# Performance work log

Hardware: AMD Instinct MI355X
Metric: run time of the kernel (lower is better)

The kernel has to match this reference:

```python
import jax, jax.numpy as jnp
import numpy as np

TOPK = 20
BN_EPS = 1e-5
NEG_SLOPE = 0.2  # DGL GAT default leaky_relu slope


def setup_inputs() -> dict:
    B, N, Ft, D = 128, 512, 64, 64
    key = jax.random.key(0)
    ks = jax.random.split(key, 6)
    return {
        "data": jax.random.normal(ks[0], (B, N, Ft), jnp.float32),
        "emb": jax.random.normal(ks[1], (N, D), jnp.float32) * 0.5,
        "fc_w": jax.random.normal(ks[2], (D, Ft), jnp.float32) * (1.0 / np.sqrt(Ft)),
        "fc_b": jnp.zeros((D,), jnp.float32),
        "attn_w": jax.random.normal(ks[3], (4 * D,), jnp.float32) * (1.0 / np.sqrt(4 * D)),
        "attn_b": jnp.zeros((), jnp.float32),
        "bn_gamma": jnp.ones((D,), jnp.float32),
        "bn_beta": jnp.zeros((D,), jnp.float32),
        "out_w": jax.random.normal(ks[4], (D,), jnp.float32) * (1.0 / np.sqrt(D)),
        "out_b": jnp.zeros((), jnp.float32),
    }


def reference(data, emb, fc_w, fc_b, attn_w, attn_b, bn_gamma, bn_beta, out_w, out_b):
    B, N, Ft = data.shape
    D = emb.shape[-1]

    # --- dynamic graph build from detached embeddings (cosine-sim topk) ---
    w = jax.lax.stop_gradient(emb)
    nrm = jnp.linalg.norm(w, axis=-1)
    cos = (w @ w.T) / (nrm[:, None] * nrm[None, :])      # [N, N]
    _, topk_idx = jax.lax.top_k(cos, TOPK)               # [N, TOPK]
    src = topk_idx.reshape(-1)                           # gated_j (message sources)
    dst = jnp.tile(jnp.arange(N), TOPK)                  # gated_i = arange(N).repeat(1,topk).flatten()

    # --- GAT layer: z = W x + b ; edge score from concat([z, emb]) at both ends ---
    z = jnp.einsum("bnf,df->bnd", data, fc_w) + fc_b     # [B, N, D]
    key_feat = jnp.concatenate([z, jnp.broadcast_to(emb, (B, N, D))], axis=-1)  # [B, N, 2D]
    a_src, a_dst = attn_w[: 2 * D], attn_w[2 * D :]
    s_src = jnp.einsum("bnd,d->bn", key_feat, a_src)
    s_dst = jnp.einsum("bnd,d->bn", key_feat, a_dst)
    e = jax.nn.leaky_relu(s_src[:, src] + s_dst[:, dst] + attn_b, NEG_SLOPE)    # [B, E]

    # segment softmax over incoming edges of each dst node (same edges every batch)
    m = jnp.full((B, N), -jnp.inf, e.dtype).at[:, dst].max(e)
    p = jnp.exp(e - m[:, dst])
    denom = jnp.zeros((B, N), e.dtype).at[:, dst].add(p)
    alpha = p / denom[:, dst]                            # [B, E]

    # scatter-aggregate messages
    h = jnp.zeros_like(z).at[:, dst].add(alpha[..., None] * z[:, src])          # [B, N, D]

    # --- trailing dense: mul by embedding, BatchNorm1d over channel D, relu, linear ---
    rst = h * emb[None]                                  # [B, N, D]
    mu = rst.mean(axis=(0, 1))
    var = rst.var(axis=(0, 1))
    rst = jax.nn.relu((rst - mu) / jnp.sqrt(var + BN_EPS) * bn_gamma + bn_beta)
    out = jnp.einsum("bnd,d->bn", rst, out_w) + out_b    # [B, N]
    return out
```

## Files before the change

### kernel.cpp

```cpp
#include <hip/hip_runtime.h>
#include <hip/hip_bf16.h>

#define NN 512
#define DD 64
#define TOPK 20
#define BB 128

__global__ __launch_bounds__(256) void k1_topk(const float* __restrict__ emb,
                                               const float* __restrict__ attn_w,
                                               int* __restrict__ topk,
                                               float* __restrict__ es_src,
                                               float* __restrict__ es_dst,
                                               double* __restrict__ gstats) {
    __shared__ float4 lds4[2048];
    const int bid = blockIdx.x, t = threadIdx.x;
    const int wid = t >> 6, lane = t & 63;
    const int i = bid * 4 + wid;
    const float4* e4 = (const float4*)emb;

    if (bid == 0 && t < 128) gstats[t] = 0.0;

    float4 wif[16];
    #pragma unroll
    for (int c = 0; c < 16; ++c) wif[c] = e4[i * 16 + c];

    double di = 0.0;
    #pragma unroll
    for (int c = 0; c < 16; ++c) {
        double wx = wif[c].x, wy = wif[c].y, wz = wif[c].z, ww = wif[c].w;
        di += wx * wx; di += wy * wy; di += wz * wz; di += ww * ww;
    }

    double dot[8] = {0,0,0,0,0,0,0,0};
    double dj [8] = {0,0,0,0,0,0,0,0};

    for (int tile = 0; tile < 4; ++tile) {
        __syncthreads();
        for (int m = t; m < 2048; m += 256) {
            const int row = m >> 4, c = m & 15;
            lds4[row * 16 + (c ^ (row & 15))] = e4[tile * 2048 + m];
        }
        __syncthreads();
        #pragma unroll
        for (int rb = 0; rb < 2; ++rb) {
            const int slot = tile * 2 + rb;
            const int rl = rb * 64 + lane;
            const int rx = rl & 15;
            #pragma unroll
            for (int c = 0; c < 16; ++c) {
                float4 v = lds4[rl * 16 + (c ^ rx)];
                float4 w = wif[c];
                double vx = v.x, vy = v.y, vz = v.z, vw = v.w;
                dot[slot] += (double)w.x * vx; dot[slot] += (double)w.y * vy;
                dot[slot] += (double)w.z * vz; dot[slot] += (double)w.w * vw;
                dj [slot] += vx * vx; dj[slot] += vy * vy; dj[slot] += vz * vz; dj[slot] += vw * vw;
            }
        }
    }

    const double nrm_i = sqrt(di);
    double v[8];
    #pragma unroll
    for (int s = 0; s < 8; ++s) v[s] = dot[s] / (nrm_i * sqrt(dj[s]));

    for (int k = 0; k < TOPK; ++k) {
        double bv = v[0]; int bs = 0;
        #pragma unroll
        for (int s = 1; s < 8; ++s) if (v[s] > bv) { bv = v[s]; bs = s; }
        int bi = bs * 64 + lane;
        #pragma unroll
        for (int off = 32; off > 0; off >>= 1) {
            double ov = __shfl_xor(bv, off);
            int    oi = __shfl_xor(bi, off);
            if (ov > bv || (ov == bv && oi < bi)) { bv = ov; bi = oi; }
        }
        if (lane == 0) topk[i * TOPK + k] = bi;
        if ((bi & 63) == lane) v[bi >> 6] = -1e300;
    }

    float wf = emb[i * 64 + lane];
    float v1 = wf * attn_w[64 + lane];
    float v2 = wf * attn_w[192 + lane];
    #pragma unroll
    for (int off = 32; off > 0; off >>= 1) {
        v1 += __shfl_xor(v1, off);
        v2 += __shfl_xor(v2, off);
    }
    if (lane == 0) { es_src[i] = v1; es_dst[i] = v2; }
}

__global__ __launch_bounds__(256) void k2_gemm(const float* __restrict__ data,
                                               const float* __restrict__ fc_w,
                                               const float* __restrict__ fc_b,
                                               const float* __restrict__ attn_w,
                                               float* __restrict__ z,
                                               float* __restrict__ zsrc,
                                               float* __restrict__ zdst) {
    __shared__ float As [64][68];
    __shared__ float WsT[64][68];
    __shared__ float redA[64][17];
    __shared__ float redB[64][17];
    const int t = threadIdx.x;
    const long r0 = (long)blockIdx.x * 64;
    const float4* data4 = (const float4*)data;
    const float4* fcw4  = (const float4*)fc_w;

    for (int m = t; m < 1024; m += 256) {
        const int r = m >> 4, c4 = m & 15;
        *(float4*)&As[r][c4 * 4] = data4[(r0 + r) * 16 + c4];
    }
    for (int m = t; m < 1024; m += 256) {
        const int d = m >> 4, f4 = m & 15;
        float4 v = fcw4[d * 16 + f4];
        WsT[f4 * 4 + 0][d] = v.x;
        WsT[f4 * 4 + 1][d] = v.y;
        WsT[f4 * 4 + 2][d] = v.z;
        WsT[f4 * 4 + 3][d] = v.w;
    }
    __syncthreads();

    const int tr = t >> 4, tc = t & 15;
    float acc[4][4] = {};
    for (int k0 = 0; k0 < 64; k0 += 4) {
        float4 a4[4], b4[4];
        #pragma unroll
        for (int i = 0; i < 4; ++i) a4[i] = *(float4*)&As[tr * 4 + i][k0];
        #pragma unroll
        for (int kk = 0; kk < 4; ++kk) b4[kk] = *(float4*)&WsT[k0 + kk][tc * 4];
        #pragma unroll
        for (int i = 0; i < 4; ++i) {
            acc[i][0] += a4[i].x * b4[0].x + a4[i].y * b4[1].x + a4[i].z * b4[2].x + a4[i].w * b4[3].x;
            acc[i][1] += a4[i].x * b4[0].y + a4[i].y * b4[1].y + a4[i].z * b4[2].y + a4[i].w * b4[3].y;
            acc[i][2] += a4[i].x * b4[0].z + a4[i].y * b4[1].z + a4[i].z * b4[2].z + a4[i].w * b4[3].z;
            acc[i][3] += a4[i].x * b4[0].w + a4[i].y * b4[1].w + a4[i].z * b4[2].w + a4[i].w * b4[3].w;
        }
    }
    float bias[4], aw0[4], aw2[4];
    #pragma unroll
    for (int j = 0; j < 4; ++j) {
        bias[j] = fc_b[tc * 4 + j];
        aw0[j]  = attn_w[tc * 4 + j];
        aw2[j]  = attn_w[128 + tc * 4 + j];
    }
    #pragma unroll
    for (int i = 0; i < 4; ++i) {
        float zb[4];
        #pragma unroll
        for (int j = 0; j < 4; ++j) zb[j] = acc[i][j] + bias[j];
        float4 vv; vv.x = zb[0]; vv.y = zb[1]; vv.z = zb[2]; vv.w = zb[3];
        *(float4*)&z[(r0 + tr * 4 + i) * 64 + tc * 4] = vv;
        redA[tr * 4 + i][tc] = zb[0] * aw0[0] + zb[1] * aw0[1] + zb[2] * aw0[2] + zb[3] * aw0[3];
        redB[tr * 4 + i][tc] = zb[0] * aw2[0] + zb[1] * aw2[1] + zb[2] * aw2[2] + zb[3] * aw2[3];
    }
    __syncthreads();
    if (t < 64) {
        float sA = 0.f, sB = 0.f;
        #pragma unroll
        for (int k = 0; k < 16; ++k) { sA += redA[t][k]; sB += redB[t][k]; }
        zsrc[r0 + t] = sA;
        zdst[r0 + t] = sB;
    }
}

__global__ __launch_bounds__(256) void k3_attn(const float* __restrict__ z,
                                               const float* __restrict__ zsrc,
                                               const float* __restrict__ zdst,
                                               const float* __restrict__ es_src,
                                               const float* __restrict__ es_dst,
                                               const int* __restrict__ topk,
                                               const float* __restrict__ emb,
                                               const float* __restrict__ attn_b_p,
                                               float* __restrict__ rst,
                                               double* __restrict__ gstats) {
    __shared__ float  zs[512 * 16];
    __shared__ double alf_pool[2560];
    __shared__ unsigned short sIdx[256 * 20];
    float* alf = (float*)alf_pool;

    const int b    = blockIdx.x >> 2;
    const int dq   = blockIdx.x & 3;
    const int doff = dq * 16;
    const int t    = threadIdx.x;
    const float attn_b = *attn_b_p;
    const long b512 = (long)b * NN;

    float4* zs4 = (float4*)zs;
    for (int m = t; m < 2048; m += 256) {
        const int n = m >> 2, c4i = m & 3;
        zs4[m] = *(const float4*)(z + (b512 + n) * 64 + doff + c4i * 4);
    }
    __syncthreads();

    const int c4 = t & 3;
    const int rq = t >> 2;
    double s1[4] = {0,0,0,0}, s2[4] = {0,0,0,0};

    for (int chunk = 0; chunk < 2; ++chunk) {
        {
            const int n = chunk * 256 + t;
            const float sd = zdst[b512 + n] + es_dst[n] + attn_b;
            float ev[TOPK];
            float m0 = -1e30f;
            #pragma unroll
            for (int tt = 0; tt < TOPK; ++tt) {
                const int s = topk[n + tt * NN];
                sIdx[t * TOPK + tt] = (unsigned short)s;
                float e = zsrc[b512 + s] + es_src[s] + sd;
                e = (e >= 0.f) ? e : 0.2f * e;
                ev[tt] = e;
                m0 = fmaxf(m0, e);
            }
            float dsum = 0.f;
            #pragma unroll
            for (int tt = 0; tt < TOPK; ++tt) { ev[tt] = __expf(ev[tt] - m0); dsum += ev[tt]; }
            const float inv = 1.0f / dsum;
            #pragma unroll
            for (int tt = 0; tt < TOPK; ++tt) alf[t * TOPK + tt] = ev[tt] * inv;
        }
        __syncthreads();

        #pragma unroll
        for (int it = 0; it < 4; ++it) {
            const int nl = it * 64 + rq;
            const int n  = chunk * 256 + nl;
            float4 acc = {0.f, 0.f, 0.f, 0.f};
            #pragma unroll
            for (int tt = 0; tt < TOPK; ++tt) {
                const float a = alf[nl * TOPK + tt];
                const float4 zv = zs4[(int)sIdx[nl * TOPK + tt] * 4 + c4];
                acc.x += a * zv.x; acc.y += a * zv.y; acc.z += a * zv.z; acc.w += a * zv.w;
            }
            const float4 ev = *(const float4*)&emb[n * 64 + doff + c4 * 4];
            float4 r;
            r.x = acc.x * ev.x; r.y = acc.y * ev.y; r.z = acc.z * ev.z; r.w = acc.w * ev.w;
            *(float4*)&rst[(b512 + n) * 64 + doff + c4 * 4] = r;
            s1[0] += (double)r.x; s2[0] += (double)r.x * (double)r.x;
            s1[1] += (double)r.y; s2[1] += (double)r.y * (double)r.y;
            s1[2] += (double)r.z; s2[2] += (double)r.z * (double)r.z;
            s1[3] += (double)r.w; s2[3] += (double)r.w * (double)r.w;
        }
        __syncthreads();
    }

    double* r1 = alf_pool;
    double* r2 = alf_pool + 1024;
    #pragma unroll
    for (int j = 0; j < 4; ++j) {
        r1[(c4 * 4 + j) * 64 + rq] = s1[j];
        r2[(c4 * 4 + j) * 64 + rq] = s2[j];
    }
    __syncthreads();
    if (t < 16) {
        double a = 0.0, bb = 0.0;
        for (int q = 0; q < 64; ++q) { a += r1[t * 64 + q]; bb += r2[t * 64 + q]; }
        atomicAdd(&gstats[doff + t], a);
        atomicAdd(&gstats[64 + doff + t], bb);
    }
}

__global__ __launch_bounds__(256) void k5_out(const float* __restrict__ rst,
                                              const double* __restrict__ gstats,
                                              const float* __restrict__ gamma,
                                              const float* __restrict__ beta,
                                              const float* __restrict__ out_w,
                                              const float* __restrict__ out_b_p,
                                              float* __restrict__ out) {
    __shared__ float scv[64], biv[64];
    const int t = threadIdx.x;
    if (t < 64) {
        const double M = (double)BB * (double)NN;
        const double s  = gstats[t];
        const double s2 = gstats[64 + t];
        const double mu  = s / M;
        const double var = s2 / M - mu * mu;
        const float scale = (float)((double)gamma[t] / sqrt(var + 1e-5));
        scv[t] = scale;
        biv[t] = beta[t] - (float)mu * scale;
    }
    __syncthreads();

    const int wid = t >> 6, lane = t & 63;
    const float sc = scv[lane], bi = biv[lane], ow = out_w[lane];
    const float ob = *out_b_p;
    const long rowbase = (long)blockIdx.x * 16 + wid * 4;
    float v[4];
    #pragma unroll
    for (int rr = 0; rr < 4; ++rr)
        v[rr] = fmaxf(rst[(rowbase + rr) * 64 + lane] * sc + bi, 0.f) * ow;
    #pragma unroll
    for (int off = 32; off > 0; off >>= 1)
        #pragma unroll
        for (int rr = 0; rr < 4; ++rr) v[rr] += __shfl_down(v[rr], off);
    if (lane == 0)
        #pragma unroll
        for (int rr = 0; rr < 4; ++rr) out[rowbase + rr] = v[rr] + ob;
}

extern "C" void kernel_launch(void* const* d_in, const int* in_sizes, int n_in,
                              void* d_out, int out_size, void* d_ws, size_t ws_size,
                              hipStream_t stream) {
    const float* data   = (const float*)d_in[0];
    const float* emb    = (const float*)d_in[1];
    const float* fc_w   = (const float*)d_in[2];
    const float* fc_b   = (const float*)d_in[3];
    const float* attn_w = (const float*)d_in[4];
    const float* attn_b = (const float*)d_in[5];
    const float* gamma  = (const float*)d_in[6];
    const float* beta   = (const float*)d_in[7];
    const float* out_w  = (const float*)d_in[8];
    const float* out_b  = (const float*)d_in[9];
    float* out = (float*)d_out;

    char* ws = (char*)d_ws;
    float*  z      = (float*) (ws + 0);
    float*  rst    = (float*) (ws + 16777216);
    float*  zsrc   = (float*) (ws + 33554432);
    float*  zdst   = (float*) (ws + 33816576);
    int*    topk   = (int*)   (ws + 34078720);
    float*  es_src = (float*) (ws + 34119680);
    float*  es_dst = (float*) (ws + 34121728);
    double* gstats = (double*)(ws + 34123776);

    k1_topk<<<128, 256, 0, stream>>>(emb, attn_w, topk, es_src, es_dst, gstats);
    k2_gemm<<<1024, 256, 0, stream>>>(data, fc_w, fc_b, attn_w, z, zsrc, zdst);
    k3_attn<<<BB * 4, 256, 0, stream>>>(z, zsrc, zdst, es_src, es_dst, topk, emb,
                                        attn_b, rst, gstats);
    k5_out<<<4096, 256, 0, stream>>>(rst, gstats, gamma, beta, out_w, out_b, out);
}
```

Measured before the change: 162.6 us.

## Fuse top-k graph build and input GEMM into one heterogeneous launch

Merges the cosine-similarity top-k kernel and the fc GEMM kernel into one launch. The first 128 blocks build the graph and the remaining 512 blocks compute z. The GEMM is rewritten as one wave per 32 rows, with fc_w columns held in registers and data broadcast through readlane, and the z·attn reductions done by wave shuffles. The top-k LDS tile switches from an XOR swizzle to padded rows. This removes one launch and overlaps the two independent stages, at the cost of a long serial FMA chain per row and heavy register use (64-float Breg).

```diff
diff --git a/kernel.cpp b/kernel.cpp
--- a/kernel.cpp
+++ b/kernel.cpp
@@ -6,159 +6,145 @@
 #define TOPK 20
 #define BB 128
 
-__global__ __launch_bounds__(256) void k1_topk(const float* __restrict__ emb,
-                                               const float* __restrict__ attn_w,
-                                               int* __restrict__ topk,
-                                               float* __restrict__ es_src,
-                                               float* __restrict__ es_dst,
-                                               double* __restrict__ gstats) {
-    __shared__ float4 lds4[2048];
+__global__ __launch_bounds__(256) void L1_fused(const float* __restrict__ data,
+                                                const float* __restrict__ emb,
+                                                const float* __restrict__ fc_w,
+                                                const float* __restrict__ fc_b,
+                                                const float* __restrict__ attn_w,
+                                                float* __restrict__ z,
+                                                float* __restrict__ zsrc,
+                                                float* __restrict__ zdst,
+                                                int* __restrict__ topk,
+                                                float* __restrict__ es_src,
+                                                float* __restrict__ es_dst,
+                                                double* __restrict__ gstats) {
+    __shared__ __align__(16) char smem[34816];
     const int bid = blockIdx.x, t = threadIdx.x;
     const int wid = t >> 6, lane = t & 63;
-    const int i = bid * 4 + wid;
-    const float4* e4 = (const float4*)emb;
-
-    if (bid == 0 && t < 128) gstats[t] = 0.0;
-
-    float4 wif[16];
-    #pragma unroll
-    for (int c = 0; c < 16; ++c) wif[c] = e4[i * 16 + c];
-
-    double di = 0.0;
-    #pragma unroll
-    for (int c = 0; c < 16; ++c) {
-        double wx = wif[c].x, wy = wif[c].y, wz = wif[c].z, ww = wif[c].w;
-        di += wx * wx; di += wy * wy; di += wz * wz; di += ww * ww;
-    }
-
-    double dot[8] = {0,0,0,0,0,0,0,0};
-    double dj [8] = {0,0,0,0,0,0,0,0};
-
-    for (int tile = 0; tile < 4; ++tile) {
+
+    if (bid < 128) {
+        float4* lds4 = (float4*)smem;
+        const int i = bid * 4 + wid;
+        const float4* e4 = (const float4*)emb;
+
+        if (bid == 0 && t < 128) gstats[t] = 0.0;
+
+        float4 wif[16];
+        #pragma unroll
+        for (int c = 0; c < 16; ++c) wif[c] = e4[i * 16 + c];
+
+        double di = 0.0;
+        #pragma unroll
+        for (int c = 0; c < 16; ++c) {
+            double wx = wif[c].x, wy = wif[c].y, wz = wif[c].z, ww = wif[c].w;
+            di += wx * wx; di += wy * wy; di += wz * wz; di += ww * ww;
+        }
+
+        double dot[8] = {0,0,0,0,0,0,0,0};
+        double dj [8] = {0,0,0,0,0,0,0,0};
+
+        for (int tile = 0; tile < 4; ++tile) {
+            __syncthreads();
+            for (int m = t; m < 2048; m += 256) {
+                const int row = m >> 4, c = m & 15;
+                lds4[row * 17 + c] = e4[tile * 2048 + m];
+            }
+            __syncthreads();
+            #pragma unroll
+            for (int rb = 0; rb < 2; ++rb) {
+                const int slot = tile * 2 + rb;
+                const int rl = rb * 64 + lane;
+                #pragma unroll
+                for (int c = 0; c < 16; ++c) {
+                    float4 v = lds4[rl * 17 + c];
+                    float4 w = wif[c];
+                    double vx = v.x, vy = v.y, vz = v.z, vw = v.w;
+                    dot[slot] += (double)w.x * vx; dot[slot] += (double)w.y * vy;
+                    dot[slot] += (double)w.z * vz; dot[slot] += (double)w.w * vw;
+                    dj [slot] += vx * vx; dj[slot] += vy * vy;
+                    dj [slot] += vz * vz; dj[slot] += vw * vw;
+                }
+            }
+        }
+
+        const double nrm_i = sqrt(di);
+        double v[8];
+        #pragma unroll
+        for (int s = 0; s < 8; ++s) v[s] = dot[s] / (nrm_i * sqrt(dj[s]));
+
+        for (int k = 0; k < TOPK; ++k) {
+            double bv = v[0]; int bs = 0;
+            #pragma unroll
+            for (int s = 1; s < 8; ++s) if (v[s] > bv) { bv = v[s]; bs = s; }
+            int bi = bs * 64 + lane;
+            #pragma unroll
+            for (int off = 32; off > 0; off >>= 1) {
+                double ov = __shfl_xor(bv, off);
+                int    oi = __shfl_xor(bi, off);
+                if (ov > bv || (ov == bv && oi < bi)) { bv = ov; bi = oi; }
+            }
+            if (lane == 0) topk[i * TOPK + k] = bi;
+            if ((bi & 63) == lane) v[bi >> 6] = -1e300;
+        }
+
+        float wf = emb[i * 64 + lane];
+        float v1 = wf * attn_w[64 + lane];
+        float v2 = wf * attn_w[192 + lane];
+        #pragma unroll
+        for (int off = 32; off > 0; off >>= 1) {
+            v1 += __shfl_xor(v1, off);
+            v2 += __shfl_xor(v2, off);
+        }
+        if (lane == 0) { es_src[i] = v1; es_dst[i] = v2; }
+    } else {
+        float* WsT = (float*)smem;
+        const float4* fcw4 = (const float4*)fc_w;
+        for (int m = t; m < 1024; m += 256) {
+            const int d = m >> 4, f4 = m & 15;
+            float4 v = fcw4[d * 16 + f4];
+            WsT[(f4 * 4 + 0) * 65 + d] = v.x;
+            WsT[(f4 * 4 + 1) * 65 + d] = v.y;
+            WsT[(f4 * 4 + 2) * 65 + d] = v.z;
+            WsT[(f4 * 4 + 3) * 65 + d] = v.w;
+        }
         __syncthreads();
-        for (int m = t; m < 2048; m += 256) {
-            const int row = m >> 4, c = m & 15;
-            lds4[row * 16 + (c ^ (row & 15))] = e4[tile * 2048 + m];
-        }
-        __syncthreads();
-        #pragma unroll
-        for (int rb = 0; rb < 2; ++rb) {
-            const int slot = tile * 2 + rb;
-            const int rl = rb * 64 + lane;
-            const int rx = rl & 15;
-            #pragma unroll
-            for (int c = 0; c < 16; ++c) {
-                float4 v = lds4[rl * 16 + (c ^ rx)];
-                float4 w = wif[c];
-                double vx = v.x, vy = v.y, vz = v.z, vw = v.w;
-                dot[slot] += (double)w.x * vx; dot[slot] += (double)w.y * vy;
-                dot[slot] += (double)w.z * vz; dot[slot] += (double)w.w * vw;
-                dj [slot] += vx * vx; dj[slot] += vy * vy; dj[slot] += vz * vz; dj[slot] += vw * vw;
-            }
-        }
-    }
-
-    const double nrm_i = sqrt(di);
-    double v[8];
-    #pragma unroll
-    for (int s = 0; s < 8; ++s) v[s] = dot[s] / (nrm_i * sqrt(dj[s]));
-
-    for (int k = 0; k < TOPK; ++k) {
-        double bv = v[0]; int bs = 0;
-        #pragma unroll
-        for (int s = 1; s < 8; ++s) if (v[s] > bv) { bv = v[s]; bs = s; }
-        int bi = bs * 64 + lane;
-        #pragma unroll
-        for (int off = 32; off > 0; off >>= 1) {
-            double ov = __shfl_xor(bv, off);
-            int    oi = __shfl_xor(bi, off);
-            if (ov > bv || (ov == bv && oi < bi)) { bv = ov; bi = oi; }
-        }
-        if (lane == 0) topk[i * TOPK + k] = bi;
-        if ((bi & 63) == lane) v[bi >> 6] = -1e300;
-    }
-
-    float wf = emb[i * 64 + lane];
-    float v1 = wf * attn_w[64 + lane];
-    float v2 = wf * attn_w[192 + lane];
-    #pragma unroll
-    for (int off = 32; off > 0; off >>= 1) {
-        v1 += __shfl_xor(v1, off);
-        v2 += __shfl_xor(v2, off);
-    }
-    if (lane == 0) { es_src[i] = v1; es_dst[i] = v2; }
-}
-
-__global__ __launch_bounds__(256) void k2_gemm(const float* __restrict__ data,
-                                               const float* __restrict__ fc_w,
-                                               const float* __restrict__ fc_b,
-                                               const float* __restrict__ attn_w,
-                                               float* __restrict__ z,
-                                               float* __restrict__ zsrc,
-                                               float* __restrict__ zdst) {
-    __shared__ float As [64][68];
-    __shared__ float WsT[64][68];
-    __shared__ float redA[64][17];
-    __shared__ float redB[64][17];
-    const int t = threadIdx.x;
-    const long r0 = (long)blockIdx.x * 64;
-    const float4* data4 = (const float4*)data;
-    const float4* fcw4  = (const float4*)fc_w;
-
-    for (int m = t; m < 1024; m += 256) {
-        const int r = m >> 4, c4 = m & 15;
-        *(float4*)&As[r][c4 * 4] = data4[(r0 + r) * 16 + c4];
-    }
-    for (int m = t; m < 1024; m += 256) {
-        const int d = m >> 4, f4 = m & 15;
-        float4 v = fcw4[d * 16 + f4];
-        WsT[f4 * 4 + 0][d] = v.x;
-        WsT[f4 * 4 + 1][d] = v.y;
-        WsT[f4 * 4 + 2][d] = v.z;
-        WsT[f4 * 4 + 3][d] = v.w;
-    }
-    __syncthreads();
-
-    const int tr = t >> 4, tc = t & 15;
-    float acc[4][4] = {};
-    for (int k0 = 0; k0 < 64; k0 += 4) {
-        float4 a4[4], b4[4];
-        #pragma unroll
-        for (int i = 0; i < 4; ++i) a4[i] = *(float4*)&As[tr * 4 + i][k0];
-        #pragma unroll
-        for (int kk = 0; kk < 4; ++kk) b4[kk] = *(float4*)&WsT[k0 + kk][tc * 4];
-        #pragma unroll
-        for (int i = 0; i < 4; ++i) {
-            acc[i][0] += a4[i].x * b4[0].x + a4[i].y * b4[1].x + a4[i].z * b4[2].x + a4[i].w * b4[3].x;
-            acc[i][1] += a4[i].x * b4[0].y + a4[i].y * b4[1].y + a4[i].z * b4[2].y + a4[i].w * b4[3].y;
-            acc[i][2] += a4[i].x * b4[0].z + a4[i].y * b4[1].z + a4[i].z * b4[2].z + a4[i].w * b4[3].z;
-            acc[i][3] += a4[i].x * b4[0].w + a4[i].y * b4[1].w + a4[i].z * b4[2].w + a4[i].w * b4[3].w;
-        }
-    }
-    float bias[4], aw0[4], aw2[4];
-    #pragma unroll
-    for (int j = 0; j < 4; ++j) {
-        bias[j] = fc_b[tc * 4 + j];
-        aw0[j]  = attn_w[tc * 4 + j];
-        aw2[j]  = attn_w[128 + tc * 4 + j];
-    }
-    #pragma unroll
-    for (int i = 0; i < 4; ++i) {
-        float zb[4];
-        #pragma unroll
-        for (int j = 0; j < 4; ++j) zb[j] = acc[i][j] + bias[j];
-        float4 vv; vv.x = zb[0]; vv.y = zb[1]; vv.z = zb[2]; vv.w = zb[3];
-        *(float4*)&z[(r0 + tr * 4 + i) * 64 + tc * 4] = vv;
-        redA[tr * 4 + i][tc] = zb[0] * aw0[0] + zb[1] * aw0[1] + zb[2] * aw0[2] + zb[3] * aw0[3];
-        redB[tr * 4 + i][tc] = zb[0] * aw2[0] + zb[1] * aw2[1] + zb[2] * aw2[2] + zb[3] * aw2[3];
-    }
-    __syncthreads();
-    if (t < 64) {
-        float sA = 0.f, sB = 0.f;
-        #pragma unroll
-        for (int k = 0; k < 16; ++k) { sA += redA[t][k]; sB += redB[t][k]; }
-        zsrc[r0 + t] = sA;
-        zdst[r0 + t] = sB;
+
+        float Breg[64];
+        #pragma unroll
+        for (int f = 0; f < 64; ++f) Breg[f] = WsT[f * 65 + lane];
+
+        const float bias = fc_b[lane];
+        const float aw0  = attn_w[lane];
+        const float aw2  = attn_w[128 + lane];
+        const long rbase = ((long)(bid - 128) * 4 + wid) * 32;
+
+        #pragma unroll
+        for (int g = 0; g < 4; ++g) {
+            float a8[8];
+            #pragma unroll
+            for (int r = 0; r < 8; ++r)
+                a8[r] = data[(rbase + g * 8 + r) * 64 + lane];
+            #pragma unroll
+            for (int r = 0; r < 8; ++r) {
+                float acc = 0.f;
+                #pragma unroll
+                for (int f = 0; f < 64; ++f) {
+                    const float af = __int_as_float(
+                        __builtin_amdgcn_readlane(__float_as_int(a8[r]), f));
+                    acc = fmaf(af, Breg[f], acc);
+                }
+                const float zb = acc + bias;
+                const long row = rbase + g * 8 + r;
+                z[row * 64 + lane] = zb;
+                float p1 = zb * aw0, p2 = zb * aw2;
+                #pragma unroll
+                for (int off = 32; off > 0; off >>= 1) {
+                    p1 += __shfl_xor(p1, off);
+                    p2 += __shfl_xor(p2, off);
+                }
+                if (lane == 0) { zsrc[row] = p1; zdst[row] = p2; }
+            }
+        }
     }
 }
 
@@ -321,8 +307,8 @@
     float*  es_dst = (float*) (ws + 34121728);
     double* gstats = (double*)(ws + 34123776);
 
-    k1_topk<<<128, 256, 0, stream>>>(emb, attn_w, topk, es_src, es_dst, gstats);
-    k2_gemm<<<1024, 256, 0, stream>>>(data, fc_w, fc_b, attn_w, z, zsrc, zdst);
+    L1_fused<<<640, 256, 0, stream>>>(data, emb, fc_w, fc_b, attn_w,
+                                      z, zsrc, zdst, topk, es_src, es_dst, gstats);
     k3_attn<<<BB * 4, 256, 0, stream>>>(z, zsrc, zdst, es_src, es_dst, topk, emb,
                                         attn_b, rst, gstats);
     k5_out<<<4096, 256, 0, stream>>>(rst, gstats, gamma, beta, out_w, out_b, out);
```

Result: faster. 156.7 us (-3.6%).
